# Optimization experiments

Measured on AMD Instinct MI355X. Metric: run time of the kernel, lower is better.

## Reference

```python
import jax, jax.numpy as jnp
import numpy as np
import math

D_MODEL = 1024
NUM_HEADS = 16
HEAD_DIM = D_MODEL // NUM_HEADS


def _xavier(key, out_f, in_f):
    limit = math.sqrt(6.0 / (in_f + out_f))
    return jax.random.uniform(key, (out_f, in_f), jnp.float32, -limit, limit)


def ternarize(w):
    # abs-mean threshold -> {-1, 0, +1}
    abs_mean = jnp.mean(jnp.abs(w))
    return jnp.where(jnp.abs(w) > abs_mean, jnp.sign(w), jnp.zeros_like(w))


def setup_inputs() -> dict:
    key = jax.random.key(0)
    kq, kk, kv, kwq, kwk, kwv, kwo = jax.random.split(key, 7)
    B, S = 2, 2048
    return {
        "query": jax.random.normal(kq, (B, S, D_MODEL), jnp.float32),
        "key": jax.random.normal(kk, (B, S, D_MODEL), jnp.float32),
        "value": jax.random.normal(kv, (B, S, D_MODEL), jnp.float32),
        "w_q": _xavier(kwq, D_MODEL, D_MODEL),
        "w_k": _xavier(kwk, D_MODEL, D_MODEL),
        "w_v": _xavier(kwv, D_MODEL, D_MODEL),
        "w_o": _xavier(kwo, D_MODEL, D_MODEL),
    }


def reference(query, key, value, w_q, w_k, w_v, w_o):
    B, S, _ = query.shape
    # ternary projections (F.linear: x @ W.T)
    q = query @ ternarize(w_q).T
    k = key @ ternarize(w_k).T
    v = value @ ternarize(w_v).T
    # [B, H, S, Dh]
    q = q.reshape(B, S, NUM_HEADS, HEAD_DIM).transpose(0, 2, 1, 3)
    k = k.reshape(B, -1, NUM_HEADS, HEAD_DIM).transpose(0, 2, 1, 3)
    v = v.reshape(B, -1, NUM_HEADS, HEAD_DIM).transpose(0, 2, 1, 3)
    scores = jnp.einsum("bhqd,bhkd->bhqk", q, k) / math.sqrt(HEAD_DIM)
    probs = jax.nn.softmax(scores, axis=-1)
    out = jnp.einsum("bhqk,bhkd->bhqd", probs, v)
    out = out.transpose(0, 2, 1, 3).reshape(B, S, D_MODEL)
    return out @ ternarize(w_o).T
```

## Files before the change

### kernel.cpp

```cpp
#include <hip/hip_runtime.h>
#include <cstdint>
#include <cstddef>

typedef __bf16 bfloat;
typedef __bf16 bf16x8 __attribute__((ext_vector_type(8)));
typedef __bf16 bf16x4 __attribute__((ext_vector_type(4)));
typedef float  f32x4  __attribute__((ext_vector_type(4)));

static constexpr int D  = 1024;
static constexpr int S  = 2048;
static constexpr int B  = 2;
static constexpr int H  = 16;
static constexpr int DH = 64;
static constexpr int M  = B * S;
static constexpr int WMAT_N = 1024 * 1024;

#define MFMA_BF16(a, b, c) __builtin_amdgcn_mfma_f32_16x16x32_bf16((a), (b), (c), 0, 0, 0)

__device__ __forceinline__ void gl_lds16(const void* g, void* l) {
  __builtin_amdgcn_global_load_lds(
      (const __attribute__((address_space(1))) void*)g,
      (__attribute__((address_space(3))) void*)l, 16, 0, 0);
}

__global__ void prep_kernel(const float* __restrict__ w0, const float* __restrict__ w1,
                            const float* __restrict__ w2, const float* __restrict__ w3,
                            const float* __restrict__ qx, const float* __restrict__ kx,
                            const float* __restrict__ vx, bfloat* __restrict__ qhi,
                            bfloat* __restrict__ qlo, bfloat* __restrict__ khi,
                            bfloat* __restrict__ klo, bfloat* __restrict__ vhi,
                            double* __restrict__ sums) {
  const int y = blockIdx.y;
  if (y < 4) {
    const float* w = (y == 0) ? w0 : (y == 1) ? w1 : (y == 2) ? w2 : w3;
    const float4* w4 = (const float4*)w;
    double s = 0.0;
    for (int i = blockIdx.x * blockDim.x + threadIdx.x; i < (WMAT_N / 4);
         i += gridDim.x * blockDim.x) {
      float4 v = w4[i];
      s += (double)fabsf(v.x) + (double)fabsf(v.y) + (double)fabsf(v.z) + (double)fabsf(v.w);
    }
    for (int off = 1; off < 64; off <<= 1) s += __shfl_xor(s, off, 64);
    __shared__ double ps[4];
    if ((threadIdx.x & 63) == 0) ps[threadIdx.x >> 6] = s;
    __syncthreads();
    if (threadIdx.x == 0) atomicAdd(&sums[y], ps[0] + ps[1] + ps[2] + ps[3]);
  } else {
    const int z = y - 4;
    const float* x = (z == 0) ? qx : (z == 1) ? kx : vx;
    bfloat* hi = (z == 0) ? qhi : (z == 1) ? khi : vhi;
    bfloat* lo = (z == 0) ? qlo : (z == 1) ? klo : nullptr;
    const int n8 = M * D / 8;
    const float4* x4 = (const float4*)x;
    for (int i = blockIdx.x * blockDim.x + threadIdx.x; i < n8;
         i += gridDim.x * blockDim.x) {
      float4 a = x4[2 * i], b = x4[2 * i + 1];
      float f[8] = {a.x, a.y, a.z, a.w, b.x, b.y, b.z, b.w};
      bf16x8 h;
#pragma unroll
      for (int j = 0; j < 8; j++) h[j] = (bfloat)f[j];
      *(bf16x8*)&hi[(size_t)i * 8] = h;
      if (z < 2) {
        bf16x8 l;
#pragma unroll
        for (int j = 0; j < 8; j++) l[j] = (bfloat)(f[j] - (float)h[j]);
        *(bf16x8*)&lo[(size_t)i * 8] = l;
      }
    }
  }
}

__global__ void tern_kernel(const float* __restrict__ w0, const float* __restrict__ w1,
                            const float* __restrict__ w2, const float* __restrict__ w3,
                            bfloat* __restrict__ o0, bfloat* __restrict__ o1,
                            bfloat* __restrict__ o2, bfloat* __restrict__ o3,
                            const double* __restrict__ sums) {
  int z = blockIdx.y;
  const float* w = (z == 0) ? w0 : (z == 1) ? w1 : (z == 2) ? w2 : w3;
  bfloat* o = (z == 0) ? o0 : (z == 1) ? o1 : (z == 2) ? o2 : o3;
  double thr = sums[z] * (1.0 / (double)WMAT_N);
  const float4* w4 = (const float4*)w;
  for (int i = blockIdx.x * blockDim.x + threadIdx.x; i < (WMAT_N / 4);
       i += gridDim.x * blockDim.x) {
    float4 v = w4[i];
    bf16x4 r;
    r[0] = (bfloat)(((double)fabsf(v.x) > thr) ? (v.x > 0.f ? 1.f : -1.f) : 0.f);
    r[1] = (bfloat)(((double)fabsf(v.y) > thr) ? (v.y > 0.f ? 1.f : -1.f) : 0.f);
    r[2] = (bfloat)(((double)fabsf(v.z) > thr) ? (v.z > 0.f ? 1.f : -1.f) : 0.f);
    r[3] = (bfloat)(((double)fabsf(v.w) > thr) ? (v.w > 0.f ? 1.f : -1.f) : 0.f);
    *(bf16x4*)&o[(size_t)i * 4] = r;
  }
}

__global__ __launch_bounds__(256) void qkv_gemm(
    const bfloat* __restrict__ xqh, const bfloat* __restrict__ xql,
    const bfloat* __restrict__ xkh, const bfloat* __restrict__ xkl,
    const bfloat* __restrict__ xvh, const bfloat* __restrict__ wqt,
    const bfloat* __restrict__ wkt, const bfloat* __restrict__ wvt,
    bfloat* __restrict__ qmh, bfloat* __restrict__ qml,
    bfloat* __restrict__ kmh, bfloat* __restrict__ kml, bfloat* __restrict__ vtr) {
  constexpr int K = D;
  constexpr int N = D;
  __shared__ __align__(16) bfloat As0[128 * 64];
  __shared__ __align__(16) bfloat As1[128 * 64];
  __shared__ __align__(16) bfloat Ws[128 * 64];

  const int z = blockIdx.z;
  const bfloat *A0, *A1 = nullptr, *Wm;
  bfloat *Oh = nullptr, *Ol = nullptr;
  float scale = 1.f;
  bool split;
  if (z == 0) {
    A0 = xqh; A1 = xql; Wm = wqt; Oh = qmh; Ol = qml;
    scale = 0.18033688f;
    split = true;
  } else if (z == 1) {
    A0 = xkh; A1 = xkl; Wm = wkt; Oh = kmh; Ol = kml; split = true;
  } else {
    A0 = xvh; Wm = wvt; split = false;
  }

  const int t = threadIdx.x;
  const int w = t >> 6, lane = t & 63;
  const int quad = lane >> 4, l16 = lane & 15;
  const int wm = w >> 1, wn = w & 1;
  const int m0 = blockIdx.y * 128, n0 = blockIdx.x * 128;

  f32x4 acc[4][4] = {};

  const int srr = lane >> 3;
  const int spc = lane & 7;

  for (int kk = 0; kk < K; kk += 64) {
#pragma unroll
    for (int g = 0; g < 4; g++) {
      int row = w * 32 + g * 8 + srr;
      int cl = spc ^ (row & 7);
      int lo = (w * 32 + g * 8) * 64;
      gl_lds16(A0 + (size_t)(m0 + row) * K + kk + cl * 8, As0 + lo);
      if (split) gl_lds16(A1 + (size_t)(m0 + row) * K + kk + cl * 8, As1 + lo);
      gl_lds16(Wm + (size_t)(n0 + row) * K + kk + cl * 8, Ws + lo);
    }
    __syncthreads();

#pragma unroll
    for (int kidx = 0; kidx < 2; kidx++) {
      bf16x8 bfrag[4], afrag[4];
#pragma unroll
      for (int nt = 0; nt < 4; nt++) {
        int r = wn * 64 + nt * 16 + l16;
        bfrag[nt] = *(const bf16x8*)&Ws[r * 64 + (((kidx * 4 + quad) ^ (r & 7)) * 8)];
      }
#pragma unroll
      for (int mt = 0; mt < 4; mt++) {
        int r = wm * 64 + mt * 16 + l16;
        afrag[mt] = *(const bf16x8*)&As0[r * 64 + (((kidx * 4 + quad) ^ (r & 7)) * 8)];
      }
#pragma unroll
      for (int mt = 0; mt < 4; mt++)
#pragma unroll
        for (int nt = 0; nt < 4; nt++)
          acc[mt][nt] = MFMA_BF16(afrag[mt], bfrag[nt], acc[mt][nt]);
      if (split) {
#pragma unroll
        for (int mt = 0; mt < 4; mt++) {
          int r = wm * 64 + mt * 16 + l16;
          afrag[mt] = *(const bf16x8*)&As1[r * 64 + (((kidx * 4 + quad) ^ (r & 7)) * 8)];
        }
#pragma unroll
        for (int mt = 0; mt < 4; mt++)
#pragma unroll
          for (int nt = 0; nt < 4; nt++)
            acc[mt][nt] = MFMA_BF16(afrag[mt], bfrag[nt], acc[mt][nt]);
      }
    }
    __syncthreads();
  }

#pragma unroll
  for (int mt = 0; mt < 4; mt++) {
#pragma unroll
    for (int nt = 0; nt < 4; nt++) {
      const int row = m0 + wm * 64 + mt * 16 + quad * 4;
      const int col = n0 + wn * 64 + nt * 16 + l16;
      if (split) {
#pragma unroll
        for (int rg = 0; rg < 4; rg++) {
          float vv = acc[mt][nt][rg] * scale;
          size_t idx = (size_t)(row + rg) * N + col;
          bfloat hh = (bfloat)vv;
          Oh[idx] = hh;
          Ol[idx] = (bfloat)(vv - (float)hh);
        }
      } else {
        int bb = row >> 11, s = row & (S - 1);
        int kk6 = s & 63;
        int pos = (kk6 & 3) | (((kk6 >> 4) & 1) << 2) | (((kk6 >> 2) & 3) << 3) |
                  ((kk6 >> 5) << 5);
        int sp = (s & ~63) | pos;
        bf16x4 pk;
#pragma unroll
        for (int rg = 0; rg < 4; rg++) pk[rg] = (bfloat)acc[mt][nt][rg];
        *(bf16x4*)&vtr[(size_t)bb * D * S + (size_t)col * S + sp] = pk;
      }
    }
  }
}

__global__ __launch_bounds__(256, 4) void gemm_wo(const bfloat* __restrict__ A,
                                                  const bfloat* __restrict__ Wm,
                                                  float* __restrict__ Cf) {
  constexpr int K = D;
  constexpr int N = D;
  __shared__ __align__(16) bfloat As[64 * 64];
  __shared__ __align__(16) bfloat Ws[64 * 64];

  const int t = threadIdx.x;
  const int w = t >> 6, lane = t & 63;
  const int quad = lane >> 4, l16 = lane & 15;
  const int wm = w >> 1, wn = w & 1;
  const int m0 = blockIdx.y * 64, n0 = blockIdx.x * 64;

  f32x4 acc[2][2] = {};

  const int srr = lane >> 3;
  const int spc = lane & 7;

  for (int kk = 0; kk < K; kk += 64) {
#pragma unroll
    for (int g = 0; g < 2; g++) {
      int row = w * 16 + g * 8 + srr;
      int cl = spc ^ (row & 7);
      int lo = (w * 16 + g * 8) * 64;
      gl_lds16(A + (size_t)(m0 + row) * K + kk + cl * 8, As + lo);
      gl_lds16(Wm + (size_t)(n0 + row) * K + kk + cl * 8, Ws + lo);
    }
    __syncthreads();

#pragma unroll
    for (int kidx = 0; kidx < 2; kidx++) {
      bf16x8 af[2], bfr[2];
#pragma unroll
      for (int i = 0; i < 2; i++) {
        int ar = wm * 32 + i * 16 + l16;
        af[i] = *(const bf16x8*)&As[ar * 64 + (((kidx * 4 + quad) ^ (ar & 7)) * 8)];
        int br = wn * 32 + i * 16 + l16;
        bfr[i] = *(const bf16x8*)&Ws[br * 64 + (((kidx * 4 + quad) ^ (br & 7)) * 8)];
      }
#pragma unroll
      for (int mt = 0; mt < 2; mt++)
#pragma unroll
        for (int nt = 0; nt < 2; nt++)
          acc[mt][nt] = MFMA_BF16(af[mt], bfr[nt], acc[mt][nt]);
    }
    __syncthreads();
  }

#pragma unroll
  for (int mt = 0; mt < 2; mt++) {
#pragma unroll
    for (int nt = 0; nt < 2; nt++) {
      const int row = m0 + wm * 32 + mt * 16 + quad * 4;
      const int col = n0 + wn * 32 + nt * 16 + l16;
#pragma unroll
      for (int rg = 0; rg < 4; rg++) Cf[(size_t)(row + rg) * N + col] = acc[mt][nt][rg];
    }
  }
}

__global__ __launch_bounds__(512) void flash_kernel(
    const bfloat* __restrict__ qh, const bfloat* __restrict__ ql,
    const bfloat* __restrict__ kh, const bfloat* __restrict__ kl,
    const bfloat* __restrict__ vt, bfloat* __restrict__ outp) {
  __shared__ __align__(16) bfloat SM[20480];

  const int tid = threadIdx.x;
  const int w = tid >> 6, lane = tid & 63;
  const int quad = lane >> 4, l16 = lane & 15;

  const int blk = blockIdx.x;
  const int xcd = blk & 7, slot = blk >> 3;
  const int g = xcd * 4 + (slot >> 4);
  const int h = g & 15, b = g >> 4;
  const int q0 = (slot & 15) * 128;

  const size_t base = (size_t)b * S * D + (size_t)h * DH;
  const size_t vbase = (size_t)b * D * S + (size_t)h * DH * S;

  const int ssr = lane >> 3;
  const int spc = lane & 7;
  const int c8 = (spc ^ ssr) * 8;
  const int stKV = w * 8 * 64;

  const bfloat* pKh = kh + base + (size_t)(w * 8 + ssr) * D + c8;
  const bfloat* pKl = kl + base + (size_t)(w * 8 + ssr) * D + c8;
  const bfloat* pV = vt + vbase + (size_t)(w * 8 + ssr) * S + c8;

  bf16x8 ones;
#pragma unroll
  for (int j = 0; j < 8; j++) ones[j] = (bfloat)1.f;

  {
    const bfloat* pQh = qh + base + (size_t)(q0 + w * 16 + ssr) * D + c8;
    const bfloat* pQl = ql + base + (size_t)(q0 + w * 16 + ssr) * D + c8;
    gl_lds16(pQh, SM + w * 1024);
    gl_lds16(pQh + 8 * D, SM + w * 1024 + 512);
    gl_lds16(pQl, SM + 8192 + w * 1024);
    gl_lds16(pQl + 8 * D, SM + 8192 + w * 1024 + 512);
  }
  asm volatile("s_waitcnt vmcnt(0)" ::: "memory");
  __builtin_amdgcn_s_barrier();
  asm volatile("" ::: "memory");

  const int fo0 = l16 * 64 + ((quad ^ (l16 & 7)) * 8);
  const int fo4 = fo0 ^ 32;
  const int fq = w * 1024;

  bf16x8 qhf0 = *(const bf16x8*)&SM[fq + fo0];
  bf16x8 qhf1 = *(const bf16x8*)&SM[fq + fo4];
  bf16x8 qlf0 = *(const bf16x8*)&SM[8192 + fq + fo0];
  bf16x8 qlf1 = *(const bf16x8*)&SM[8192 + fq + fo4];
  asm volatile("s_waitcnt lgkmcnt(0)" ::: "memory");
  __builtin_amdgcn_s_barrier();
  asm volatile("" ::: "memory");

  gl_lds16(pKh, SM + 0 + stKV);
  gl_lds16(pKl, SM + 4096 + stKV);
  pKh += 64 * D;
  pKl += 64 * D;
  asm volatile("s_waitcnt vmcnt(0)" ::: "memory");

  f32x4 Oa[4] = {};
  f32x4 La = {};
  float m_i = -3.0e38f;
  constexpr int NT = S / 64;

  for (int t = 0; t < NT; ++t) {
    __builtin_amdgcn_s_barrier();
    asm volatile("" ::: "memory");
    const int cur = (t & 1) * 8192;
    const int nxt = 8192 - cur;

    gl_lds16(pV, SM + 16384 + stKV);
    pV += 64;
    if (t < NT - 1) {
      gl_lds16(pKh, SM + nxt + stKV);
      gl_lds16(pKl, SM + nxt + 4096 + stKV);
      pKh += 64 * D;
      pKl += 64 * D;
    }

    f32x4 sf[4];
    __builtin_amdgcn_s_setprio(1);
#pragma unroll
    for (int mt = 0; mt < 4; mt++) {
      f32x4 a = {};
      bf16x8 bh0 = *(const bf16x8*)&SM[cur + fo0 + mt * 1024];
      bf16x8 bl0 = *(const bf16x8*)&SM[cur + 4096 + fo0 + mt * 1024];
      bf16x8 bh1 = *(const bf16x8*)&SM[cur + fo4 + mt * 1024];
      bf16x8 bl1 = *(const bf16x8*)&SM[cur + 4096 + fo4 + mt * 1024];
      a = MFMA_BF16(bh0, qhf0, a);
      a = MFMA_BF16(bl0, qhf0, a);
      a = MFMA_BF16(bh0, qlf0, a);
      a = MFMA_BF16(bh1, qhf1, a);
      a = MFMA_BF16(bl1, qhf1, a);
      a = MFMA_BF16(bh1, qlf1, a);
      sf[mt] = a;
    }
    __builtin_amdgcn_s_setprio(0);

    float t0 = fmaxf(fmaxf(sf[0][0], sf[0][1]), fmaxf(sf[0][2], sf[0][3]));
    float t1 = fmaxf(fmaxf(sf[1][0], sf[1][1]), fmaxf(sf[1][2], sf[1][3]));
    float t2 = fmaxf(fmaxf(sf[2][0], sf[2][1]), fmaxf(sf[2][2], sf[2][3]));
    float t3 = fmaxf(fmaxf(sf[3][0], sf[3][1]), fmaxf(sf[3][2], sf[3][3]));
    float mm = fmaxf(fmaxf(t0, t1), fmaxf(t2, t3));
    mm = fmaxf(mm, __shfl_xor(mm, 16, 64));
    mm = fmaxf(mm, __shfl_xor(mm, 32, 64));
    if (__ballot(mm > m_i + 8.0f)) {
      float mnew = fmaxf(m_i, mm);
      float alpha = exp2f(m_i - mnew);
      m_i = mnew;
#pragma unroll
      for (int mt = 0; mt < 4; mt++) Oa[mt] *= alpha;
      La *= alpha;
    }
#pragma unroll
    for (int mt = 0; mt < 4; mt++)
#pragma unroll
      for (int rg = 0; rg < 4; rg++) sf[mt][rg] = exp2f(sf[mt][rg] - m_i);

    if (t < NT - 1)
      asm volatile("s_waitcnt vmcnt(2)" ::: "memory");
    else
      asm volatile("s_waitcnt vmcnt(0)" ::: "memory");
    __builtin_amdgcn_s_barrier();
    asm volatile("" ::: "memory");

    __builtin_amdgcn_s_setprio(1);
#pragma unroll
    for (int kp = 0; kp < 2; kp++) {
      bf16x8 pb8;
#pragma unroll
      for (int rg = 0; rg < 4; rg++) {
        pb8[rg] = (bfloat)sf[2 * kp][rg];
        pb8[4 + rg] = (bfloat)sf[2 * kp + 1][rg];
      }
      La = MFMA_BF16(ones, pb8, La);
      const int fv = kp ? fo4 : fo0;
#pragma unroll
      for (int mt = 0; mt < 4; mt++) {
        bf16x8 va = *(const bf16x8*)&SM[16384 + fv + mt * 1024];
        Oa[mt] = MFMA_BF16(va, pb8, Oa[mt]);
      }
    }
    __builtin_amdgcn_s_setprio(0);
    asm volatile("s_waitcnt vmcnt(0)" ::: "memory");
  }

  float inv = 1.0f / La[0];
  const int qrow = q0 + w * 16 + l16;
#pragma unroll
  for (int mt = 0; mt < 4; mt++) {
    bf16x4 ov;
#pragma unroll
    for (int rg = 0; rg < 4; rg++) ov[rg] = (bfloat)(Oa[mt][rg] * inv);
    *(bf16x4*)&outp[base + (size_t)qrow * D + mt * 16 + quad * 4] = ov;
  }
}

extern "C" void kernel_launch(void* const* d_in, const int* in_sizes, int n_in,
                              void* d_out, int out_size, void* d_ws, size_t ws_size,
                              hipStream_t stream) {
  const float* q_in = (const float*)d_in[0];
  const float* k_in = (const float*)d_in[1];
  const float* v_in = (const float*)d_in[2];
  const float* wq = (const float*)d_in[3];
  const float* wk = (const float*)d_in[4];
  const float* wv = (const float*)d_in[5];
  const float* wo = (const float*)d_in[6];
  float* outp = (float*)d_out;
  char* ws = (char*)d_ws;

  constexpr size_t WBYTES = (size_t)WMAT_N * 2;
  constexpr size_t XBYTES = (size_t)M * D * 2;
  size_t off = 0;
  double* sums = (double*)(ws + off); off += 256;
  bfloat* wqt = (bfloat*)(ws + off); off += WBYTES;
  bfloat* wkt = (bfloat*)(ws + off); off += WBYTES;
  bfloat* wvt = (bfloat*)(ws + off); off += WBYTES;
  bfloat* wot = (bfloat*)(ws + off); off += WBYTES;
  bfloat* xqh = (bfloat*)(ws + off); off += XBYTES;
  bfloat* xql = (bfloat*)(ws + off); off += XBYTES;
  bfloat* xkh = (bfloat*)(ws + off); off += XBYTES;
  bfloat* xkl = (bfloat*)(ws + off); off += XBYTES;
  bfloat* xvh = (bfloat*)(ws + off); off += XBYTES;
  bfloat* qmh = (bfloat*)(ws + off); off += XBYTES;
  bfloat* qml = (bfloat*)(ws + off); off += XBYTES;
  bfloat* kmh = (bfloat*)(ws + off); off += XBYTES;
  bfloat* kml = (bfloat*)(ws + off); off += XBYTES;
  bfloat* vtr = (bfloat*)(ws + off); off += XBYTES;
  bfloat* attn = xqh;

  hipMemsetAsync(sums, 0, 4 * sizeof(double), stream);
  prep_kernel<<<dim3(256, 7), 256, 0, stream>>>(
      wq, wk, wv, wo, q_in, k_in, v_in, xqh, xql, xkh, xkl, xvh, sums);
  tern_kernel<<<dim3(128, 4), 256, 0, stream>>>(wq, wk, wv, wo, wqt, wkt, wvt, wot, sums);
  qkv_gemm<<<dim3(D / 128, M / 128, 3), 256, 0, stream>>>(
      xqh, xql, xkh, xkl, xvh, wqt, wkt, wvt, qmh, qml, kmh, kml, vtr);
  flash_kernel<<<512, 512, 0, stream>>>(qmh, qml, kmh, kml, vtr, attn);
  gemm_wo<<<dim3(D / 64, M / 64), 256, 0, stream>>>(attn, wot, outp);
}
```

Measured before the change: 279.9 us.

## Give each flash-attention wave two query tiles with half the waves per block

The flash attention kernel now runs 4 waves per block instead of 8, and each wave processes two 16-row query sub-tiles. Every K and V fragment read from LDS is reused across both sub-tiles, which halves LDS read traffic per MFMA. Each wave also issues twice as many global-to-LDS loads, and the vmcnt wait is adjusted to match. The cost is roughly doubled accumulator and score register use per wave and fewer waves available to hide latency.

```diff
diff --git a/kernel.cpp b/kernel.cpp
--- a/kernel.cpp
+++ b/kernel.cpp
@@ -268,7 +268,7 @@
   }
 }
 
-__global__ __launch_bounds__(512) void flash_kernel(
+__global__ __launch_bounds__(256) void flash_kernel(
     const bfloat* __restrict__ qh, const bfloat* __restrict__ ql,
     const bfloat* __restrict__ kh, const bfloat* __restrict__ kl,
     const bfloat* __restrict__ vt, bfloat* __restrict__ outp) {
@@ -290,23 +290,24 @@
   const int ssr = lane >> 3;
   const int spc = lane & 7;
   const int c8 = (spc ^ ssr) * 8;
-  const int stKV = w * 8 * 64;
-
-  const bfloat* pKh = kh + base + (size_t)(w * 8 + ssr) * D + c8;
-  const bfloat* pKl = kl + base + (size_t)(w * 8 + ssr) * D + c8;
-  const bfloat* pV = vt + vbase + (size_t)(w * 8 + ssr) * S + c8;
+  const int stKV = w * 1024;
+
+  const bfloat* pKh = kh + base + (size_t)(w * 16 + ssr) * D + c8;
+  const bfloat* pKl = kl + base + (size_t)(w * 16 + ssr) * D + c8;
+  const bfloat* pV = vt + vbase + (size_t)(w * 16 + ssr) * S + c8;
 
   bf16x8 ones;
 #pragma unroll
   for (int j = 0; j < 8; j++) ones[j] = (bfloat)1.f;
 
   {
-    const bfloat* pQh = qh + base + (size_t)(q0 + w * 16 + ssr) * D + c8;
-    const bfloat* pQl = ql + base + (size_t)(q0 + w * 16 + ssr) * D + c8;
-    gl_lds16(pQh, SM + w * 1024);
-    gl_lds16(pQh + 8 * D, SM + w * 1024 + 512);
-    gl_lds16(pQl, SM + 8192 + w * 1024);
-    gl_lds16(pQl + 8 * D, SM + 8192 + w * 1024 + 512);
+    const bfloat* pQh = qh + base + (size_t)(q0 + w * 32 + ssr) * D + c8;
+    const bfloat* pQl = ql + base + (size_t)(q0 + w * 32 + ssr) * D + c8;
+#pragma unroll
+    for (int gq = 0; gq < 4; gq++) {
+      gl_lds16(pQh + gq * 8 * D, SM + w * 2048 + gq * 512);
+      gl_lds16(pQl + gq * 8 * D, SM + 8192 + w * 2048 + gq * 512);
+    }
   }
   asm volatile("s_waitcnt vmcnt(0)" ::: "memory");
   __builtin_amdgcn_s_barrier();
@@ -314,25 +315,31 @@
 
   const int fo0 = l16 * 64 + ((quad ^ (l16 & 7)) * 8);
   const int fo4 = fo0 ^ 32;
-  const int fq = w * 1024;
-
-  bf16x8 qhf0 = *(const bf16x8*)&SM[fq + fo0];
-  bf16x8 qhf1 = *(const bf16x8*)&SM[fq + fo4];
-  bf16x8 qlf0 = *(const bf16x8*)&SM[8192 + fq + fo0];
-  bf16x8 qlf1 = *(const bf16x8*)&SM[8192 + fq + fo4];
+
+  bf16x8 qhf[2][2], qlf[2][2];
+#pragma unroll
+  for (int qs = 0; qs < 2; qs++) {
+    const int fq = w * 2048 + qs * 1024;
+    qhf[qs][0] = *(const bf16x8*)&SM[fq + fo0];
+    qhf[qs][1] = *(const bf16x8*)&SM[fq + fo4];
+    qlf[qs][0] = *(const bf16x8*)&SM[8192 + fq + fo0];
+    qlf[qs][1] = *(const bf16x8*)&SM[8192 + fq + fo4];
+  }
   asm volatile("s_waitcnt lgkmcnt(0)" ::: "memory");
   __builtin_amdgcn_s_barrier();
   asm volatile("" ::: "memory");
 
   gl_lds16(pKh, SM + 0 + stKV);
+  gl_lds16(pKh + 8 * D, SM + 0 + stKV + 512);
   gl_lds16(pKl, SM + 4096 + stKV);
+  gl_lds16(pKl + 8 * D, SM + 4096 + stKV + 512);
   pKh += 64 * D;
   pKl += 64 * D;
   asm volatile("s_waitcnt vmcnt(0)" ::: "memory");
 
-  f32x4 Oa[4] = {};
-  f32x4 La = {};
-  float m_i = -3.0e38f;
+  f32x4 Oa[2][4] = {};
+  f32x4 La[2] = {};
+  float m_i[2] = {-3.0e38f, -3.0e38f};
   constexpr int NT = S / 64;
 
   for (int t = 0; t < NT; ++t) {
@@ -342,55 +349,64 @@
     const int nxt = 8192 - cur;
 
     gl_lds16(pV, SM + 16384 + stKV);
+    gl_lds16(pV + 8 * S, SM + 16384 + stKV + 512);
     pV += 64;
     if (t < NT - 1) {
       gl_lds16(pKh, SM + nxt + stKV);
+      gl_lds16(pKh + 8 * D, SM + nxt + stKV + 512);
       gl_lds16(pKl, SM + nxt + 4096 + stKV);
+      gl_lds16(pKl + 8 * D, SM + nxt + 4096 + stKV + 512);
       pKh += 64 * D;
       pKl += 64 * D;
     }
 
-    f32x4 sf[4];
+    f32x4 sf[2][4];
     __builtin_amdgcn_s_setprio(1);
 #pragma unroll
     for (int mt = 0; mt < 4; mt++) {
-      f32x4 a = {};
       bf16x8 bh0 = *(const bf16x8*)&SM[cur + fo0 + mt * 1024];
       bf16x8 bl0 = *(const bf16x8*)&SM[cur + 4096 + fo0 + mt * 1024];
       bf16x8 bh1 = *(const bf16x8*)&SM[cur + fo4 + mt * 1024];
       bf16x8 bl1 = *(const bf16x8*)&SM[cur + 4096 + fo4 + mt * 1024];
-      a = MFMA_BF16(bh0, qhf0, a);
-      a = MFMA_BF16(bl0, qhf0, a);
-      a = MFMA_BF16(bh0, qlf0, a);
-      a = MFMA_BF16(bh1, qhf1, a);
-      a = MFMA_BF16(bl1, qhf1, a);
-      a = MFMA_BF16(bh1, qlf1, a);
-      sf[mt] = a;
+#pragma unroll
+      for (int qs = 0; qs < 2; qs++) {
+        f32x4 a = {};
+        a = MFMA_BF16(bh0, qhf[qs][0], a);
+        a = MFMA_BF16(bl0, qhf[qs][0], a);
+        a = MFMA_BF16(bh0, qlf[qs][0], a);
+        a = MFMA_BF16(bh1, qhf[qs][1], a);
+        a = MFMA_BF16(bl1, qhf[qs][1], a);
+        a = MFMA_BF16(bh1, qlf[qs][1], a);
+        sf[qs][mt] = a;
+      }
     }
     __builtin_amdgcn_s_setprio(0);
 
-    float t0 = fmaxf(fmaxf(sf[0][0], sf[0][1]), fmaxf(sf[0][2], sf[0][3]));
-    float t1 = fmaxf(fmaxf(sf[1][0], sf[1][1]), fmaxf(sf[1][2], sf[1][3]));
-    float t2 = fmaxf(fmaxf(sf[2][0], sf[2][1]), fmaxf(sf[2][2], sf[2][3]));
-    float t3 = fmaxf(fmaxf(sf[3][0], sf[3][1]), fmaxf(sf[3][2], sf[3][3]));
-    float mm = fmaxf(fmaxf(t0, t1), fmaxf(t2, t3));
-    mm = fmaxf(mm, __shfl_xor(mm, 16, 64));
-    mm = fmaxf(mm, __shfl_xor(mm, 32, 64));
-    if (__ballot(mm > m_i + 8.0f)) {
-      float mnew = fmaxf(m_i, mm);
-      float alpha = exp2f(m_i - mnew);
-      m_i = mnew;
-#pragma unroll
-      for (int mt = 0; mt < 4; mt++) Oa[mt] *= alpha;
-      La *= alpha;
-    }
-#pragma unroll
-    for (int mt = 0; mt < 4; mt++)
-#pragma unroll
-      for (int rg = 0; rg < 4; rg++) sf[mt][rg] = exp2f(sf[mt][rg] - m_i);
+#pragma unroll
+    for (int qs = 0; qs < 2; qs++) {
+      float t0 = fmaxf(fmaxf(sf[qs][0][0], sf[qs][0][1]), fmaxf(sf[qs][0][2], sf[qs][0][3]));
+      float t1 = fmaxf(fmaxf(sf[qs][1][0], sf[qs][1][1]), fmaxf(sf[qs][1][2], sf[qs][1][3]));
+      float t2 = fmaxf(fmaxf(sf[qs][2][0], sf[qs][2][1]), fmaxf(sf[qs][2][2], sf[qs][2][3]));
+      float t3 = fmaxf(fmaxf(sf[qs][3][0], sf[qs][3][1]), fmaxf(sf[qs][3][2], sf[qs][3][3]));
+      float mm = fmaxf(fmaxf(t0, t1), fmaxf(t2, t3));
+      mm = fmaxf(mm, __shfl_xor(mm, 16, 64));
+      mm = fmaxf(mm, __shfl_xor(mm, 32, 64));
+      if (__ballot(mm > m_i[qs] + 8.0f)) {
+        float mnew = fmaxf(m_i[qs], mm);
+        float alpha = exp2f(m_i[qs] - mnew);
+        m_i[qs] = mnew;
+#pragma unroll
+        for (int mt = 0; mt < 4; mt++) Oa[qs][mt] *= alpha;
+        La[qs] *= alpha;
+      }
+#pragma unroll
+      for (int mt = 0; mt < 4; mt++)
+#pragma unroll
+        for (int rg = 0; rg < 4; rg++) sf[qs][mt][rg] = exp2f(sf[qs][mt][rg] - m_i[qs]);
+    }
 
     if (t < NT - 1)
-      asm volatile("s_waitcnt vmcnt(2)" ::: "memory");
+      asm volatile("s_waitcnt vmcnt(4)" ::: "memory");
     else
       asm volatile("s_waitcnt vmcnt(0)" ::: "memory");
     __builtin_amdgcn_s_barrier();
@@ -399,32 +415,39 @@
     __builtin_amdgcn_s_setprio(1);
 #pragma unroll
     for (int kp = 0; kp < 2; kp++) {
-      bf16x8 pb8;
-#pragma unroll
-      for (int rg = 0; rg < 4; rg++) {
-        pb8[rg] = (bfloat)sf[2 * kp][rg];
-        pb8[4 + rg] = (bfloat)sf[2 * kp + 1][rg];
-      }
-      La = MFMA_BF16(ones, pb8, La);
+      bf16x8 pb8[2];
+#pragma unroll
+      for (int qs = 0; qs < 2; qs++) {
+#pragma unroll
+        for (int rg = 0; rg < 4; rg++) {
+          pb8[qs][rg] = (bfloat)sf[qs][2 * kp][rg];
+          pb8[qs][4 + rg] = (bfloat)sf[qs][2 * kp + 1][rg];
+        }
+        La[qs] = MFMA_BF16(ones, pb8[qs], La[qs]);
+      }
       const int fv = kp ? fo4 : fo0;
 #pragma unroll
       for (int mt = 0; mt < 4; mt++) {
         bf16x8 va = *(const bf16x8*)&SM[16384 + fv + mt * 1024];
-        Oa[mt] = MFMA_BF16(va, pb8, Oa[mt]);
+        Oa[0][mt] = MFMA_BF16(va, pb8[0], Oa[0][mt]);
+        Oa[1][mt] = MFMA_BF16(va, pb8[1], Oa[1][mt]);
       }
     }
     __builtin_amdgcn_s_setprio(0);
     asm volatile("s_waitcnt vmcnt(0)" ::: "memory");
   }
 
-  float inv = 1.0f / La[0];
-  const int qrow = q0 + w * 16 + l16;
-#pragma unroll
-  for (int mt = 0; mt < 4; mt++) {
-    bf16x4 ov;
-#pragma unroll
-    for (int rg = 0; rg < 4; rg++) ov[rg] = (bfloat)(Oa[mt][rg] * inv);
-    *(bf16x4*)&outp[base + (size_t)qrow * D + mt * 16 + quad * 4] = ov;
+#pragma unroll
+  for (int qs = 0; qs < 2; qs++) {
+    float inv = 1.0f / La[qs][0];
+    const int qrow = q0 + w * 32 + qs * 16 + l16;
+#pragma unroll
+    for (int mt = 0; mt < 4; mt++) {
+      bf16x4 ov;
+#pragma unroll
+      for (int rg = 0; rg < 4; rg++) ov[rg] = (bfloat)(Oa[qs][mt][rg] * inv);
+      *(bf16x4*)&outp[base + (size_t)qrow * D + mt * 16 + quad * 4] = ov;
+    }
   }
 }
 
@@ -467,6 +490,6 @@
   tern_kernel<<<dim3(128, 4), 256, 0, stream>>>(wq, wk, wv, wo, wqt, wkt, wvt, wot, sums);
   qkv_gemm<<<dim3(D / 128, M / 128, 3), 256, 0, stream>>>(
       xqh, xql, xkh, xkl, xvh, wqt, wkt, wvt, qmh, qml, kmh, kml, vtr);
-  flash_kernel<<<512, 512, 0, stream>>>(qmh, qml, kmh, kml, vtr, attn);
+  flash_kernel<<<512, 256, 0, stream>>>(qmh, qml, kmh, kml, vtr, attn);
   gemm_wo<<<dim3(D / 64, M / 64), 256, 0, stream>>>(attn, wot, outp);
 }
```

Result: slower. 291.1 us (+4.0%).
